# Kernel optimization log

Hardware: AMD Instinct MI355X
Metric: run time of the kernel (lower is better)

## Reference

```python
import jax, jax.numpy as jnp
import numpy as np

EMBED_DIM = 1024
HEADS = 16
HD = EMBED_DIM // HEADS

def setup_inputs() -> dict:
    key = jax.random.key(0)
    ks = jax.random.split(key, 6)
    s = 1.0 / np.sqrt(EMBED_DIM)
    x = jax.random.normal(ks[0], (4, 2048, EMBED_DIM), dtype=jnp.float32)
    Wq = jax.random.uniform(ks[1], (EMBED_DIM, EMBED_DIM), jnp.float32, -s, s)
    Wk = jax.random.uniform(ks[2], (EMBED_DIM, EMBED_DIM), jnp.float32, -s, s)
    Wv = jax.random.uniform(ks[3], (EMBED_DIM, EMBED_DIM), jnp.float32, -s, s)
    Wo = jax.random.uniform(ks[4], (EMBED_DIM, EMBED_DIM), jnp.float32, -s, s)
    bo = jax.random.uniform(ks[5], (EMBED_DIM,), jnp.float32, -s, s)
    return {"x": x, "Wq": Wq, "Wk": Wk, "Wv": Wv, "Wo": Wo, "bo": bo}

def reference(x, Wq, Wk, Wv, Wo, bo):
    B, S, E = x.shape
    # projections (torch Linear: y = x @ W.T), split into heads -> [B,H,S,hd]
    def proj(W):
        return (x @ W.T).reshape(B, S, HEADS, HD).transpose(0, 2, 1, 3)
    q, k, v = proj(Wq), proj(Wk), proj(Wv)
    energy = jnp.einsum('bhid,bhjd->bhij', q, k) / np.sqrt(HD).astype(np.float32)
    causal = jnp.tril(jnp.ones((S, S), dtype=bool))
    energy = jnp.where(causal, energy, -jnp.inf)
    attn = jax.nn.softmax(energy, axis=-1)  # dropout omitted (eval mode)
    out = jnp.einsum('bhij,bhjd->bhid', attn, v)
    out = out.transpose(0, 2, 1, 3).reshape(B, S, E)
    return out @ Wo.T + bo
```

## Files before the change

kernel.cpp:

```cpp
#include <hip/hip_runtime.h>
#include <math.h>

#define EMB   1024
#define HEADS 16
#define HD    64
#define SEQ   2048
#define BATCH 4
#define MTOT  (BATCH * SEQ)
#define XSZ   ((size_t)MTOT * EMB)
#define WSZ   ((size_t)EMB * EMB)

typedef __attribute__((ext_vector_type(8))) short s16x8;
typedef __attribute__((ext_vector_type(4))) short s16x4;
typedef __attribute__((ext_vector_type(4))) float f32x4;

__device__ __forceinline__ short f2bf(float f) {
    unsigned u = __builtin_bit_cast(unsigned, f);
    u += 0x7fffu + ((u >> 16) & 1u);
    return (short)(u >> 16);
}

__device__ __forceinline__ unsigned pk_bf16(float a, float b) {
#if __has_builtin(__builtin_amdgcn_cvt_pk_bf16_f32)
    typedef __attribute__((ext_vector_type(2))) __bf16 bf16x2;
    return __builtin_bit_cast(unsigned, __builtin_amdgcn_cvt_pk_bf16_f32(a, b));
#else
    return (unsigned)(unsigned short)f2bf(a) |
           ((unsigned)(unsigned short)f2bf(b) << 16);
#endif
}

__device__ __forceinline__ float fexp2(float x) {
#if __has_builtin(__builtin_amdgcn_exp2f)
    return __builtin_amdgcn_exp2f(x);
#else
    return exp2f(x);
#endif
}

__device__ __forceinline__ void async16(const void* g, void* l) {
    __builtin_amdgcn_global_load_lds(
        (const __attribute__((address_space(1))) unsigned*)g,
        (__attribute__((address_space(3))) unsigned*)l, 16, 0, 0);
}

__global__ __launch_bounds__(256)
void cvt_inputs(const float* __restrict__ x,  const float* __restrict__ wq,
                const float* __restrict__ wk, const float* __restrict__ wv,
                const float* __restrict__ wo, short* __restrict__ xb,
                short* __restrict__ wcat)
{
    const size_t e = ((size_t)blockIdx.x * 256 + threadIdx.x) * 8;
    const float* src;
    short* dst;
    float scale = 1.0f;
    if (e < XSZ) {
        src = x + e;
        dst = xb + e;
    } else {
        const size_t r = e - XSZ;
        const int w = (int)(r >> 20);
        const size_t off = r & (WSZ - 1);
        src = (w == 0 ? wq : w == 1 ? wk : w == 2 ? wv : wo) + off;
        dst = wcat + r;
        if (w == 0) scale = 0.125f * 1.44269504f;
    }
    const float4 a = ((const float4*)src)[0];
    const float4 b = ((const float4*)src)[1];
    s16x8 v;
    v[0] = f2bf(a.x * scale); v[1] = f2bf(a.y * scale);
    v[2] = f2bf(a.z * scale); v[3] = f2bf(a.w * scale);
    v[4] = f2bf(b.x * scale); v[5] = f2bf(b.y * scale);
    v[6] = f2bf(b.z * scale); v[7] = f2bf(b.w * scale);
    *(s16x8*)dst = v;
}

#define BAR() __builtin_amdgcn_s_barrier()
#define WAIT_LGKM() do { asm volatile("s_waitcnt lgkmcnt(0)" ::: "memory"); \
                         __builtin_amdgcn_sched_barrier(0); } while (0)
#define WAIT_VM(n) asm volatile("s_waitcnt vmcnt(" #n ")" ::: "memory")

#define RD_A4(bA) \
    _Pragma("unroll") for (int mi = 0; mi < 4; ++mi) \
    _Pragma("unroll") for (int kk = 0; kk < 2; ++kk) \
        a[mi][kk] = *(const s16x8*)((bA) + (wm4 + mi) * 2048 + kk * 1024 + abase);

#define RD_B2(bB, hf, breg) \
    _Pragma("unroll") for (int ni = 0; ni < 2; ++ni) \
    _Pragma("unroll") for (int kk = 0; kk < 2; ++kk) \
        breg[ni][kk] = *(const s16x8*)((bB) + (wn4 + (hf) * 2 + ni) * 2048 + kk * 1024 + abase);

#define MFMA16(hf, breg) \
    __builtin_amdgcn_s_setprio(1); \
    _Pragma("unroll") for (int mi = 0; mi < 4; ++mi) \
    _Pragma("unroll") for (int ni = 0; ni < 2; ++ni) \
    _Pragma("unroll") for (int kk = 0; kk < 2; ++kk) \
        acc[mi][(hf) * 2 + ni] = __builtin_amdgcn_mfma_f32_16x16x32_bf16( \
            a[mi][kk], breg[ni][kk], acc[mi][(hf) * 2 + ni], 0, 0, 0); \
    __builtin_amdgcn_s_setprio(0);

#define STA(pM, ldsM, h, k0) do { \
    async16((pM) + (size_t)((h) * 128) * K + (k0),      (ldsM) + (h) * 16384 + wv1024); \
    async16((pM) + (size_t)((h) * 128 + 64) * K + (k0), (ldsM) + (h) * 16384 + 8192 + wv1024); \
} while (0)

#define STB(pM, ldsM, k0) do { \
    async16((pM) + (k0),                (ldsM) + wv1024); \
    async16((pM) + (size_t)64 * K + (k0), (ldsM) + 8192 + wv1024); \
} while (0)

template<bool OUT_BF16>
__global__ __launch_bounds__(512, 2)
void gemm_qp(const short* __restrict__ A, const short* __restrict__ B,
             void* __restrict__ C, int ldc, const float* __restrict__ bias,
             int K, short* __restrict__ Vt)
{
    __shared__ __align__(16) char lds[147456];

    const int tid   = threadIdx.x;
    const int wv    = tid >> 6;
    const int lane  = tid & 63;
    const int col16 = lane & 15;
    const int quad  = lane >> 4;
    const int wm    = wv >> 1;
    const int wn    = wv & 1;
    const int wm4   = wm * 4;
    const int wn4   = wn * 4;
    const int wv1024 = wv << 10;

    const int nwg = gridDim.x * gridDim.y;
    int wg = blockIdx.y * gridDim.x + blockIdx.x;
    wg = (wg & 7) * (nwg >> 3) + (wg >> 3);
    const int rowBase = (wg / gridDim.x) * 256;
    const int colBase = (wg % gridDim.x) * 128;

    const int abase = (col16 * 64 + quad * 16) ^ ((col16 & 8) << 2);

    const int rlane = (lane >> 2) & 15;
    const int rw0   = ((wv >> 1) << 4) + rlane;
    const int colSt = ((wv & 1) << 5) + (((lane & 3) << 3) ^ ((lane & 32) >> 1));
    const short* pA = A + (size_t)(rowBase + rw0) * K + colSt;
    const short* pB = B + (size_t)(colBase + rw0) * K + colSt;

    s16x8 a[4][2], bq0[2][2], bq1[2][2];
    f32x4 acc[4][4];
#pragma unroll
    for (int i = 0; i < 4; ++i)
#pragma unroll
        for (int j = 0; j < 4; ++j) acc[i][j] = (f32x4){0.f, 0.f, 0.f, 0.f};

    const int NT = K >> 6;

    char* r0 = lds;
    char* r1 = lds + 49152;
    char* r2 = lds + 98304;

    STA(pA, r0, 0, 0);  STA(pA, r0, 1, 0);  STB(pB, r0 + 32768, 0);
    STA(pA, r1, 0, 64); STA(pA, r1, 1, 64); STB(pB, r1 + 32768, 64);
    WAIT_VM(6);
    BAR();

    for (int kt = 0; kt < NT; ++kt) {
        const int k0 = kt << 6;
        const bool more = (kt + 2 < NT);

        RD_A4(r0);
        RD_B2(r0 + 32768, 0, bq0);
        if (more) { STA(pA, r2, 0, k0 + 128); STB(pB, r2 + 32768, k0 + 128); }
        BAR(); WAIT_LGKM();
        MFMA16(0, bq0);
        BAR();

        RD_B2(r0 + 32768, 1, bq1);
        if (more) STA(pA, r2, 1, k0 + 128);
        BAR(); WAIT_LGKM();
        MFMA16(1, bq1);
        if (more) { WAIT_VM(6); } else { WAIT_VM(0); }
        BAR();

        char* t = r0; r0 = r1; r1 = r2; r2 = t;
    }

    if (OUT_BF16) {
        short* Cb = (short*)C;
        if (Vt != nullptr && colBase >= 2048) {
#pragma unroll
            for (int mi = 0; mi < 4; ++mi) {
                const int rg0 = rowBase + wm * 64 + mi * 16 + quad * 4;
                const int bq = rg0 >> 11;
                const int s0 = rg0 & 2047;
#pragma unroll
                for (int ni = 0; ni < 4; ++ni) {
                    const int cg2 = colBase - 2048 + wn * 64 + ni * 16 + col16;
                    const int hh = cg2 >> 6, dd = cg2 & 63;
                    short* dst = Vt + (((size_t)(bq * 16 + hh) * 64 + dd) << 11) + s0;
                    const f32x4 v = acc[mi][ni];
                    uint2 pw;
                    pw.x = pk_bf16(v[0], v[1]);
                    pw.y = pk_bf16(v[2], v[3]);
                    *(uint2*)dst = pw;
                }
            }
        } else {
#pragma unroll
            for (int mi = 0; mi < 4; ++mi) {
                const int rg0 = rowBase + wm * 64 + mi * 16 + quad * 4;
#pragma unroll
                for (int ni = 0; ni < 4; ++ni) {
                    const int cg = colBase + wn * 64 + ni * 16 + col16;
                    const f32x4 v = acc[mi][ni];
#pragma unroll
                    for (int r = 0; r < 4; ++r)
                        Cb[(size_t)(rg0 + r) * ldc + cg] = f2bf(v[r]);
                }
            }
        }
    } else {
        float* Cf = (float*)C;
#pragma unroll
        for (int ni = 0; ni < 4; ++ni) {
            const int cg = colBase + wn * 64 + ni * 16 + col16;
            const float bj = bias ? bias[cg] : 0.f;
#pragma unroll
            for (int mi = 0; mi < 4; ++mi) {
                const int rg0 = rowBase + wm * 64 + mi * 16 + quad * 4;
                const f32x4 v = acc[mi][ni];
#pragma unroll
                for (int r = 0; r < 4; ++r)
                    Cf[(size_t)(rg0 + r) * ldc + cg] = v[r] + bj;
            }
        }
    }
}

#define LDT 2048
__global__ __launch_bounds__(512)
void attn_mfma(const short* __restrict__ QK, const short* __restrict__ VT,
               short* __restrict__ O)
{
    __shared__ __align__(16) short lKV[4][2][64 * 64];
    __shared__ short lP[8 * 32 * 64];

    char* lPc = (char*)lP;

    const int tid  = threadIdx.x;
    const int wv   = tid >> 6;
    const int lane = tid & 63;
    const int col  = lane & 15;
    const int quad = lane >> 4;
    const int csw  = (col & 7) << 4;

    const int bh = blockIdx.y;
    const int b  = bh >> 4;
    const int h  = bh & 15;
    const size_t baseq = (size_t)b * SEQ * LDT + (size_t)h * HD;
    const size_t basek = baseq + 1024;
    const size_t baseo = (size_t)b * SEQ * EMB + (size_t)h * HD;
    const short* vtb = VT + ((size_t)bh << 17);

    const int srow   = tid >> 3;
    const int schunk = tid & 7;
    const int ssc    = (schunk ^ (srow & 7)) * 8;
    const int sdst   = srow * 128 + schunk * 16;

    char* pwv = lPc + wv * 4096;

    const s16x8 onesv = {0x3F80, 0x3F80, 0x3F80, 0x3F80,
                         0x3F80, 0x3F80, 0x3F80, 0x3F80};

#define STG(kt, bi) do { \
    async16(QK + basek + (size_t)((kt) * 64 + srow) * LDT + ssc, (char*)lKV[bi][0] + sdst); \
    async16(vtb + (size_t)srow * LDT + (kt) * 64 + ssc,          (char*)lKV[bi][1] + sdst); \
} while (0)

    for (int half = 0; half < 2; ++half) {
        const int qsuper = half ? (7 - (int)blockIdx.x) : (int)blockIdx.x;
        const int qb = qsuper * 256;
        const int qlo_w = qb + wv * 32;

        s16x8 qf[2][2];
#pragma unroll
        for (int rb = 0; rb < 2; ++rb) {
            const short* qr = QK + baseq + (size_t)(qlo_w + rb * 16 + col) * LDT;
            qf[rb][0] = *(const s16x8*)(qr + quad * 8);
            qf[rb][1] = *(const s16x8*)(qr + 32 + quad * 8);
        }

        f32x4 of[2][4], lsum[2];
#pragma unroll
        for (int rb = 0; rb < 2; ++rb) {
#pragma unroll
            for (int u = 0; u < 4; ++u) of[rb][u] = (f32x4){0.f, 0.f, 0.f, 0.f};
            lsum[rb] = (f32x4){0.f, 0.f, 0.f, 0.f};
        }

        const int nt = qb / 64 + 4;

        BAR();
        STG(0, 0);
        STG(1, 1);

        for (int kt = 0; kt < nt; ++kt) {
            const int kb = kt * 64;
            const int bi = kt & 3;
            if (kt + 2 < nt) STG(kt + 2, (kt + 2) & 3);
            const int rem = nt - 1 - kt;
            if (rem >= 2)      { WAIT_VM(4); }
            else if (rem == 1) { WAIT_VM(2); }
            else               { WAIT_VM(0); }
            BAR();

            if (kb > qlo_w + 31) continue;

            const char* lKb = (const char*)lKV[bi][0];
            const char* lVb = (const char*)lKV[bi][1];

            s16x8 kf[4][2];
#pragma unroll
            for (int t = 0; t < 4; ++t) {
                kf[t][0] = *(const s16x8*)(lKb + (t * 16 + col) * 128 + ((quad * 16) ^ csw));
                kf[t][1] = *(const s16x8*)(lKb + (t * 16 + col) * 128 + ((64 + quad * 16) ^ csw));
            }

#pragma unroll
            for (int rb = 0; rb < 2; ++rb) {
                const int qlo = qlo_w + rb * 16;
                const int qg  = qlo + col;

                f32x4 s[4];
#pragma unroll
                for (int t = 0; t < 4; ++t) {
                    f32x4 acc = (f32x4){0.f, 0.f, 0.f, 0.f};
                    acc = __builtin_amdgcn_mfma_f32_16x16x32_bf16(kf[t][0], qf[rb][0], acc, 0, 0, 0);
                    acc = __builtin_amdgcn_mfma_f32_16x16x32_bf16(kf[t][1], qf[rb][1], acc, 0, 0, 0);
                    s[t] = acc;
                }

                if (kb + 63 > qlo) {
#pragma unroll
                    for (int t = 0; t < 4; ++t)
#pragma unroll
                        for (int rr = 0; rr < 4; ++rr) {
                            const int kg = kb + t * 16 + quad * 4 + rr;
                            if (kg > qg) s[t][rr] = -3.0e38f;
                        }
                }

                char* pb = pwv + (rb * 16 + col) * 128;
#pragma unroll
                for (int t = 0; t < 4; ++t) {
                    uint2 pkd;
                    pkd.x = pk_bf16(fexp2(s[t][0]), fexp2(s[t][1]));
                    pkd.y = pk_bf16(fexp2(s[t][2]), fexp2(s[t][3]));
                    *(uint2*)(pb + ((t * 32 + quad * 8) ^ csw)) = pkd;
                }
            }

#pragma unroll
            for (int c = 0; c < 2; ++c) {
                s16x8 vf[4];
#pragma unroll
                for (int u = 0; u < 4; ++u)
                    vf[u] = *(const s16x8*)(lVb + (u * 16 + col) * 128 + ((c * 64 + quad * 16) ^ csw));
#pragma unroll
                for (int rb = 0; rb < 2; ++rb) {
                    const s16x8 pa = *(const s16x8*)(pwv + (rb * 16 + col) * 128 + ((c * 64 + quad * 16) ^ csw));
                    lsum[rb] = __builtin_amdgcn_mfma_f32_16x16x32_bf16(onesv, pa, lsum[rb], 0, 0, 0);
#pragma unroll
                    for (int u = 0; u < 4; ++u)
                        of[rb][u] = __builtin_amdgcn_mfma_f32_16x16x32_bf16(vf[u], pa, of[rb][u], 0, 0, 0);
                }
            }
        }

#pragma unroll
        for (int rb = 0; rb < 2; ++rb) {
            const float rl = 1.f / lsum[rb][0];
            short* orow = O + baseo + (size_t)(qlo_w + rb * 16 + col) * EMB + quad * 4;
#pragma unroll
            for (int u = 0; u < 4; ++u) {
                uint2 pkd;
                pkd.x = pk_bf16(of[rb][u][0] * rl, of[rb][u][1] * rl);
                pkd.y = pk_bf16(of[rb][u][2] * rl, of[rb][u][3] * rl);
                *(uint2*)&orow[u * 16] = pkd;
            }
        }
    }
#undef STG
}

extern "C" void kernel_launch(void* const* d_in, const int* in_sizes, int n_in,
                              void* d_out, int out_size, void* d_ws, size_t ws_size,
                              hipStream_t stream)
{
    const float* x  = (const float*)d_in[0];
    const float* Wq = (const float*)d_in[1];
    const float* Wk = (const float*)d_in[2];
    const float* Wv = (const float*)d_in[3];
    const float* Wo = (const float*)d_in[4];
    const float* bo = (const float*)d_in[5];
    float* out = (float*)d_out;

    short* xb   = (short*)d_ws;
    short* wcat = xb + XSZ;
    short* qk   = wcat + 4 * WSZ;
    short* vt   = qk + (size_t)MTOT * 2048;
    short* ob   = vt + (size_t)64 * 64 * 2048;

    const int cvt_blocks = (int)((XSZ + 4 * WSZ) / 8 / 256);
    cvt_inputs<<<cvt_blocks, 256, 0, stream>>>(x, Wq, Wk, Wv, Wo, xb, wcat);

    gemm_qp<true><<<dim3(3072 / 128, MTOT / 256), 512, 0, stream>>>(
        xb, wcat, qk, 2048, nullptr, EMB, vt);

    attn_mfma<<<dim3(4, BATCH * HEADS), 512, 0, stream>>>(qk, vt, ob);

    gemm_qp<false><<<dim3(EMB / 128, MTOT / 256), 512, 0, stream>>>(
        ob, wcat + (size_t)3 * WSZ, out, EMB, bo, EMB, nullptr);
}
```

Before: 243.9 us.

## Split QKV GEMM into small-LDS K32 kernel and halve attention query tile

Adds a dedicated QKV projection GEMM that uses a K-step of 32 with double buffering in 48KB of LDS instead of a triple-buffered 144KB layout, so more workgroups can be resident per CU. The output-projection GEMM keeps the old pipeline as its own kernel. The attention kernel now gives each wave 16 query rows instead of 32, doubles the grid to 8 blocks per head, and uses three rotating K/V LDS buffers with a simpler wait scheme. The aim is more occupancy and better load balance, at the cost of shorter MFMA runs, more barriers per K, and less K/V reuse across query rows.

```diff
diff --git a/kernel.cpp b/kernel.cpp
--- a/kernel.cpp
+++ b/kernel.cpp
@@ -80,42 +80,17 @@
                          __builtin_amdgcn_sched_barrier(0); } while (0)
 #define WAIT_VM(n) asm volatile("s_waitcnt vmcnt(" #n ")" ::: "memory")
 
-#define RD_A4(bA) \
-    _Pragma("unroll") for (int mi = 0; mi < 4; ++mi) \
-    _Pragma("unroll") for (int kk = 0; kk < 2; ++kk) \
-        a[mi][kk] = *(const s16x8*)((bA) + (wm4 + mi) * 2048 + kk * 1024 + abase);
-
-#define RD_B2(bB, hf, breg) \
-    _Pragma("unroll") for (int ni = 0; ni < 2; ++ni) \
-    _Pragma("unroll") for (int kk = 0; kk < 2; ++kk) \
-        breg[ni][kk] = *(const s16x8*)((bB) + (wn4 + (hf) * 2 + ni) * 2048 + kk * 1024 + abase);
-
-#define MFMA16(hf, breg) \
-    __builtin_amdgcn_s_setprio(1); \
-    _Pragma("unroll") for (int mi = 0; mi < 4; ++mi) \
-    _Pragma("unroll") for (int ni = 0; ni < 2; ++ni) \
-    _Pragma("unroll") for (int kk = 0; kk < 2; ++kk) \
-        acc[mi][(hf) * 2 + ni] = __builtin_amdgcn_mfma_f32_16x16x32_bf16( \
-            a[mi][kk], breg[ni][kk], acc[mi][(hf) * 2 + ni], 0, 0, 0); \
-    __builtin_amdgcn_s_setprio(0);
-
-#define STA(pM, ldsM, h, k0) do { \
-    async16((pM) + (size_t)((h) * 128) * K + (k0),      (ldsM) + (h) * 16384 + wv1024); \
-    async16((pM) + (size_t)((h) * 128 + 64) * K + (k0), (ldsM) + (h) * 16384 + 8192 + wv1024); \
+#define STG32(dst, k0) do { \
+    async16(pA32 + (k0),                     (dst) + wv1024); \
+    async16(pA32 + (size_t)128 * EMB + (k0), (dst) + 8192 + wv1024); \
+    async16(pB32 + (k0),                     (dst) + 16384 + wv1024); \
 } while (0)
 
-#define STB(pM, ldsM, k0) do { \
-    async16((pM) + (k0),                (ldsM) + wv1024); \
-    async16((pM) + (size_t)64 * K + (k0), (ldsM) + 8192 + wv1024); \
-} while (0)
-
-template<bool OUT_BF16>
 __global__ __launch_bounds__(512, 2)
-void gemm_qp(const short* __restrict__ A, const short* __restrict__ B,
-             void* __restrict__ C, int ldc, const float* __restrict__ bias,
-             int K, short* __restrict__ Vt)
+void gemm_qkv32(const short* __restrict__ A, const short* __restrict__ B,
+                short* __restrict__ C, int ldc, short* __restrict__ Vt)
 {
-    __shared__ __align__(16) char lds[147456];
+    __shared__ __align__(16) char lds[49152];
 
     const int tid   = threadIdx.x;
     const int wv    = tid >> 6;
@@ -137,6 +112,141 @@
     const int abase = (col16 * 64 + quad * 16) ^ ((col16 & 8) << 2);
 
     const int rlane = (lane >> 2) & 15;
+    const int colSt = ((lane & 3) << 3) ^ ((lane & 32) >> 1);
+    const short* pA32 = A + (size_t)(rowBase + wv * 16 + rlane) * EMB + colSt;
+    const short* pB32 = B + (size_t)(colBase + wv * 16 + rlane) * EMB + colSt;
+
+    s16x8 a[4], bq[4];
+    f32x4 acc[4][4];
+#pragma unroll
+    for (int i = 0; i < 4; ++i)
+#pragma unroll
+        for (int j = 0; j < 4; ++j) acc[i][j] = (f32x4){0.f, 0.f, 0.f, 0.f};
+
+    char* cb = lds;
+    char* nb = lds + 24576;
+
+    STG32(cb, 0);
+
+    for (int kt = 0; kt < 32; ++kt) {
+        const int k0 = kt << 5;
+        const bool more = (kt + 1 < 32);
+
+        if (more) STG32(nb, k0 + 32);
+        if (more) { WAIT_VM(3); } else { WAIT_VM(0); }
+        BAR();
+
+#pragma unroll
+        for (int mi = 0; mi < 4; ++mi)
+            a[mi] = *(const s16x8*)(cb + (wm4 + mi) * 1024 + abase);
+#pragma unroll
+        for (int ni = 0; ni < 4; ++ni)
+            bq[ni] = *(const s16x8*)(cb + 16384 + (wn4 + ni) * 1024 + abase);
+        WAIT_LGKM();
+
+        __builtin_amdgcn_s_setprio(1);
+#pragma unroll
+        for (int mi = 0; mi < 4; ++mi)
+#pragma unroll
+            for (int ni = 0; ni < 4; ++ni)
+                acc[mi][ni] = __builtin_amdgcn_mfma_f32_16x16x32_bf16(
+                    a[mi], bq[ni], acc[mi][ni], 0, 0, 0);
+        __builtin_amdgcn_s_setprio(0);
+        BAR();
+
+        char* t = cb; cb = nb; nb = t;
+    }
+
+    if (colBase >= 2048) {
+#pragma unroll
+        for (int mi = 0; mi < 4; ++mi) {
+            const int rg0 = rowBase + wm * 64 + mi * 16 + quad * 4;
+            const int bq_ = rg0 >> 11;
+            const int s0 = rg0 & 2047;
+#pragma unroll
+            for (int ni = 0; ni < 4; ++ni) {
+                const int cg2 = colBase - 2048 + wn * 64 + ni * 16 + col16;
+                const int hh = cg2 >> 6, dd = cg2 & 63;
+                short* dst = Vt + (((size_t)(bq_ * 16 + hh) * 64 + dd) << 11) + s0;
+                const f32x4 v = acc[mi][ni];
+                uint2 pw;
+                pw.x = pk_bf16(v[0], v[1]);
+                pw.y = pk_bf16(v[2], v[3]);
+                *(uint2*)dst = pw;
+            }
+        }
+    } else {
+#pragma unroll
+        for (int mi = 0; mi < 4; ++mi) {
+            const int rg0 = rowBase + wm * 64 + mi * 16 + quad * 4;
+#pragma unroll
+            for (int ni = 0; ni < 4; ++ni) {
+                const int cg = colBase + wn * 64 + ni * 16 + col16;
+                const f32x4 v = acc[mi][ni];
+#pragma unroll
+                for (int r = 0; r < 4; ++r)
+                    C[(size_t)(rg0 + r) * ldc + cg] = f2bf(v[r]);
+            }
+        }
+    }
+}
+
+#define RD_A4(bA) \
+    _Pragma("unroll") for (int mi = 0; mi < 4; ++mi) \
+    _Pragma("unroll") for (int kk = 0; kk < 2; ++kk) \
+        a[mi][kk] = *(const s16x8*)((bA) + (wm4 + mi) * 2048 + kk * 1024 + abase);
+
+#define RD_B2(bB, hf, breg) \
+    _Pragma("unroll") for (int ni = 0; ni < 2; ++ni) \
+    _Pragma("unroll") for (int kk = 0; kk < 2; ++kk) \
+        breg[ni][kk] = *(const s16x8*)((bB) + (wn4 + (hf) * 2 + ni) * 2048 + kk * 1024 + abase);
+
+#define MFMA16(hf, breg) \
+    __builtin_amdgcn_s_setprio(1); \
+    _Pragma("unroll") for (int mi = 0; mi < 4; ++mi) \
+    _Pragma("unroll") for (int ni = 0; ni < 2; ++ni) \
+    _Pragma("unroll") for (int kk = 0; kk < 2; ++kk) \
+        acc[mi][(hf) * 2 + ni] = __builtin_amdgcn_mfma_f32_16x16x32_bf16( \
+            a[mi][kk], breg[ni][kk], acc[mi][(hf) * 2 + ni], 0, 0, 0); \
+    __builtin_amdgcn_s_setprio(0);
+
+#define STA(pM, ldsM, h, k0) do { \
+    async16((pM) + (size_t)((h) * 128) * K + (k0),      (ldsM) + (h) * 16384 + wv1024); \
+    async16((pM) + (size_t)((h) * 128 + 64) * K + (k0), (ldsM) + (h) * 16384 + 8192 + wv1024); \
+} while (0)
+
+#define STB(pM, ldsM, k0) do { \
+    async16((pM) + (k0),                (ldsM) + wv1024); \
+    async16((pM) + (size_t)64 * K + (k0), (ldsM) + 8192 + wv1024); \
+} while (0)
+
+__global__ __launch_bounds__(512, 2)
+void gemm_out(const short* __restrict__ A, const short* __restrict__ B,
+              float* __restrict__ C, int ldc, const float* __restrict__ bias,
+              int K)
+{
+    __shared__ __align__(16) char lds[147456];
+
+    const int tid   = threadIdx.x;
+    const int wv    = tid >> 6;
+    const int lane  = tid & 63;
+    const int col16 = lane & 15;
+    const int quad  = lane >> 4;
+    const int wm    = wv >> 1;
+    const int wn    = wv & 1;
+    const int wm4   = wm * 4;
+    const int wn4   = wn * 4;
+    const int wv1024 = wv << 10;
+
+    const int nwg = gridDim.x * gridDim.y;
+    int wg = blockIdx.y * gridDim.x + blockIdx.x;
+    wg = (wg & 7) * (nwg >> 3) + (wg >> 3);
+    const int rowBase = (wg / gridDim.x) * 256;
+    const int colBase = (wg % gridDim.x) * 128;
+
+    const int abase = (col16 * 64 + quad * 16) ^ ((col16 & 8) << 2);
+
+    const int rlane = (lane >> 2) & 15;
     const int rw0   = ((wv >> 1) << 4) + rlane;
     const int colSt = ((wv & 1) << 5) + (((lane & 3) << 3) ^ ((lane & 32) >> 1));
     const short* pA = A + (size_t)(rowBase + rw0) * K + colSt;
@@ -181,54 +291,17 @@
         char* t = r0; r0 = r1; r1 = r2; r2 = t;
     }
 
-    if (OUT_BF16) {
-        short* Cb = (short*)C;
-        if (Vt != nullptr && colBase >= 2048) {
-#pragma unroll
-            for (int mi = 0; mi < 4; ++mi) {
-                const int rg0 = rowBase + wm * 64 + mi * 16 + quad * 4;
-                const int bq = rg0 >> 11;
-                const int s0 = rg0 & 2047;
-#pragma unroll
-                for (int ni = 0; ni < 4; ++ni) {
-                    const int cg2 = colBase - 2048 + wn * 64 + ni * 16 + col16;
-                    const int hh = cg2 >> 6, dd = cg2 & 63;
-                    short* dst = Vt + (((size_t)(bq * 16 + hh) * 64 + dd) << 11) + s0;
-                    const f32x4 v = acc[mi][ni];
-                    uint2 pw;
-                    pw.x = pk_bf16(v[0], v[1]);
-                    pw.y = pk_bf16(v[2], v[3]);
-                    *(uint2*)dst = pw;
-                }
-            }
-        } else {
-#pragma unroll
-            for (int mi = 0; mi < 4; ++mi) {
-                const int rg0 = rowBase + wm * 64 + mi * 16 + quad * 4;
-#pragma unroll
-                for (int ni = 0; ni < 4; ++ni) {
-                    const int cg = colBase + wn * 64 + ni * 16 + col16;
-                    const f32x4 v = acc[mi][ni];
-#pragma unroll
-                    for (int r = 0; r < 4; ++r)
-                        Cb[(size_t)(rg0 + r) * ldc + cg] = f2bf(v[r]);
-                }
-            }
-        }
-    } else {
-        float* Cf = (float*)C;
-#pragma unroll
-        for (int ni = 0; ni < 4; ++ni) {
-            const int cg = colBase + wn * 64 + ni * 16 + col16;
-            const float bj = bias ? bias[cg] : 0.f;
-#pragma unroll
-            for (int mi = 0; mi < 4; ++mi) {
-                const int rg0 = rowBase + wm * 64 + mi * 16 + quad * 4;
-                const f32x4 v = acc[mi][ni];
-#pragma unroll
-                for (int r = 0; r < 4; ++r)
-                    Cf[(size_t)(rg0 + r) * ldc + cg] = v[r] + bj;
-            }
+#pragma unroll
+    for (int ni = 0; ni < 4; ++ni) {
+        const int cg = colBase + wn * 64 + ni * 16 + col16;
+        const float bj = bias ? bias[cg] : 0.f;
+#pragma unroll
+        for (int mi = 0; mi < 4; ++mi) {
+            const int rg0 = rowBase + wm * 64 + mi * 16 + quad * 4;
+            const f32x4 v = acc[mi][ni];
+#pragma unroll
+            for (int r = 0; r < 4; ++r)
+                C[(size_t)(rg0 + r) * ldc + cg] = v[r] + bj;
         }
     }
 }
@@ -238,8 +311,8 @@
 void attn_mfma(const short* __restrict__ QK, const short* __restrict__ VT,
                short* __restrict__ O)
 {
-    __shared__ __align__(16) short lKV[4][2][64 * 64];
-    __shared__ short lP[8 * 32 * 64];
+    __shared__ __align__(16) short lKV[3][2][64 * 64];
+    __shared__ __align__(16) short lP[8 * 16 * 64];
 
     char* lPc = (char*)lP;
 
@@ -250,6 +323,7 @@
     const int quad = lane >> 4;
     const int csw  = (col & 7) << 4;
 
+    const int qpair = (int)blockIdx.x;
     const int bh = blockIdx.y;
     const int b  = bh >> 4;
     const int h  = bh & 15;
@@ -263,80 +337,73 @@
     const int ssc    = (schunk ^ (srow & 7)) * 8;
     const int sdst   = srow * 128 + schunk * 16;
 
-    char* pwv = lPc + wv * 4096;
+    char* pwv = lPc + wv * 2048;
 
     const s16x8 onesv = {0x3F80, 0x3F80, 0x3F80, 0x3F80,
                          0x3F80, 0x3F80, 0x3F80, 0x3F80};
 
-#define STG(kt, bi) do { \
-    async16(QK + basek + (size_t)((kt) * 64 + srow) * LDT + ssc, (char*)lKV[bi][0] + sdst); \
-    async16(vtb + (size_t)srow * LDT + (kt) * 64 + ssc,          (char*)lKV[bi][1] + sdst); \
+#define STG(kt, bp) do { \
+    async16(QK + basek + (size_t)((kt) * 64 + srow) * LDT + ssc, (char*)((bp)[0]) + sdst); \
+    async16(vtb + (size_t)srow * LDT + (kt) * 64 + ssc,          (char*)((bp)[1]) + sdst); \
 } while (0)
 
     for (int half = 0; half < 2; ++half) {
-        const int qsuper = half ? (7 - (int)blockIdx.x) : (int)blockIdx.x;
-        const int qb = qsuper * 256;
-        const int qlo_w = qb + wv * 32;
-
-        s16x8 qf[2][2];
-#pragma unroll
-        for (int rb = 0; rb < 2; ++rb) {
-            const short* qr = QK + baseq + (size_t)(qlo_w + rb * 16 + col) * LDT;
-            qf[rb][0] = *(const s16x8*)(qr + quad * 8);
-            qf[rb][1] = *(const s16x8*)(qr + 32 + quad * 8);
-        }
-
-        f32x4 of[2][4], lsum[2];
-#pragma unroll
-        for (int rb = 0; rb < 2; ++rb) {
-#pragma unroll
-            for (int u = 0; u < 4; ++u) of[rb][u] = (f32x4){0.f, 0.f, 0.f, 0.f};
-            lsum[rb] = (f32x4){0.f, 0.f, 0.f, 0.f};
-        }
-
-        const int nt = qb / 64 + 4;
+        const int qx = half ? (15 - qpair) : qpair;
+        const int qb = qx * 128;
+        const int qlo_w = qb + wv * 16;
+
+        s16x8 qf[2];
+        {
+            const short* qr = QK + baseq + (size_t)(qlo_w + col) * LDT;
+            qf[0] = *(const s16x8*)(qr + quad * 8);
+            qf[1] = *(const s16x8*)(qr + 32 + quad * 8);
+        }
+
+        f32x4 of[4], lsum;
+#pragma unroll
+        for (int u = 0; u < 4; ++u) of[u] = (f32x4){0.f, 0.f, 0.f, 0.f};
+        lsum = (f32x4){0.f, 0.f, 0.f, 0.f};
+
+        const int nt = qb / 64 + 2;
+
+        short (*b0)[64 * 64] = lKV[0];
+        short (*b1)[64 * 64] = lKV[1];
+        short (*b2)[64 * 64] = lKV[2];
 
         BAR();
-        STG(0, 0);
-        STG(1, 1);
+        __builtin_amdgcn_sched_barrier(0);
+        STG(0, b0);
+        STG(1, b1);
 
         for (int kt = 0; kt < nt; ++kt) {
             const int kb = kt * 64;
-            const int bi = kt & 3;
-            if (kt + 2 < nt) STG(kt + 2, (kt + 2) & 3);
-            const int rem = nt - 1 - kt;
-            if (rem >= 2)      { WAIT_VM(4); }
-            else if (rem == 1) { WAIT_VM(2); }
-            else               { WAIT_VM(0); }
+            if (kt + 1 < nt) { WAIT_VM(2); } else { WAIT_VM(0); }
             BAR();
-
-            if (kb > qlo_w + 31) continue;
-
-            const char* lKb = (const char*)lKV[bi][0];
-            const char* lVb = (const char*)lKV[bi][1];
-
-            s16x8 kf[4][2];
-#pragma unroll
-            for (int t = 0; t < 4; ++t) {
-                kf[t][0] = *(const s16x8*)(lKb + (t * 16 + col) * 128 + ((quad * 16) ^ csw));
-                kf[t][1] = *(const s16x8*)(lKb + (t * 16 + col) * 128 + ((64 + quad * 16) ^ csw));
-            }
-
-#pragma unroll
-            for (int rb = 0; rb < 2; ++rb) {
-                const int qlo = qlo_w + rb * 16;
-                const int qg  = qlo + col;
+            __builtin_amdgcn_sched_barrier(0);
+            if (kt + 2 < nt) STG(kt + 2, b2);
+
+            if (kb <= qlo_w + 15) {
+                const char* lKb = (const char*)(b0[0]);
+                const char* lVb = (const char*)(b0[1]);
+
+                s16x8 kf[4][2];
+#pragma unroll
+                for (int t = 0; t < 4; ++t) {
+                    kf[t][0] = *(const s16x8*)(lKb + (t * 16 + col) * 128 + ((quad * 16) ^ csw));
+                    kf[t][1] = *(const s16x8*)(lKb + (t * 16 + col) * 128 + ((64 + quad * 16) ^ csw));
+                }
 
                 f32x4 s[4];
 #pragma unroll
                 for (int t = 0; t < 4; ++t) {
                     f32x4 acc = (f32x4){0.f, 0.f, 0.f, 0.f};
-                    acc = __builtin_amdgcn_mfma_f32_16x16x32_bf16(kf[t][0], qf[rb][0], acc, 0, 0, 0);
-                    acc = __builtin_amdgcn_mfma_f32_16x16x32_bf16(kf[t][1], qf[rb][1], acc, 0, 0, 0);
+                    acc = __builtin_amdgcn_mfma_f32_16x16x32_bf16(kf[t][0], qf[0], acc, 0, 0, 0);
+                    acc = __builtin_amdgcn_mfma_f32_16x16x32_bf16(kf[t][1], qf[1], acc, 0, 0, 0);
                     s[t] = acc;
                 }
 
-                if (kb + 63 > qlo) {
+                const int qg = qlo_w + col;
+                if (kb + 63 > qlo_w) {
 #pragma unroll
                     for (int t = 0; t < 4; ++t)
 #pragma unroll
@@ -346,7 +413,7 @@
                         }
                 }
 
-                char* pb = pwv + (rb * 16 + col) * 128;
+                char* pb = pwv + col * 128;
 #pragma unroll
                 for (int t = 0; t < 4; ++t) {
                     uint2 pkd;
@@ -354,36 +421,32 @@
                     pkd.y = pk_bf16(fexp2(s[t][2]), fexp2(s[t][3]));
                     *(uint2*)(pb + ((t * 32 + quad * 8) ^ csw)) = pkd;
                 }
-            }
-
-#pragma unroll
-            for (int c = 0; c < 2; ++c) {
-                s16x8 vf[4];
-#pragma unroll
-                for (int u = 0; u < 4; ++u)
-                    vf[u] = *(const s16x8*)(lVb + (u * 16 + col) * 128 + ((c * 64 + quad * 16) ^ csw));
-#pragma unroll
-                for (int rb = 0; rb < 2; ++rb) {
-                    const s16x8 pa = *(const s16x8*)(pwv + (rb * 16 + col) * 128 + ((c * 64 + quad * 16) ^ csw));
-                    lsum[rb] = __builtin_amdgcn_mfma_f32_16x16x32_bf16(onesv, pa, lsum[rb], 0, 0, 0);
+
+#pragma unroll
+                for (int c = 0; c < 2; ++c) {
+                    s16x8 vf[4];
 #pragma unroll
                     for (int u = 0; u < 4; ++u)
-                        of[rb][u] = __builtin_amdgcn_mfma_f32_16x16x32_bf16(vf[u], pa, of[rb][u], 0, 0, 0);
+                        vf[u] = *(const s16x8*)(lVb + (u * 16 + col) * 128 + ((c * 64 + quad * 16) ^ csw));
+                    const s16x8 pa = *(const s16x8*)(pwv + col * 128 + ((c * 64 + quad * 16) ^ csw));
+                    lsum = __builtin_amdgcn_mfma_f32_16x16x32_bf16(onesv, pa, lsum, 0, 0, 0);
+#pragma unroll
+                    for (int u = 0; u < 4; ++u)
+                        of[u] = __builtin_amdgcn_mfma_f32_16x16x32_bf16(vf[u], pa, of[u], 0, 0, 0);
                 }
             }
-        }
-
-#pragma unroll
-        for (int rb = 0; rb < 2; ++rb) {
-            const float rl = 1.f / lsum[rb][0];
-            short* orow = O + baseo + (size_t)(qlo_w + rb * 16 + col) * EMB + quad * 4;
-#pragma unroll
-            for (int u = 0; u < 4; ++u) {
-                uint2 pkd;
-                pkd.x = pk_bf16(of[rb][u][0] * rl, of[rb][u][1] * rl);
-                pkd.y = pk_bf16(of[rb][u][2] * rl, of[rb][u][3] * rl);
-                *(uint2*)&orow[u * 16] = pkd;
-            }
+
+            short (*tmp)[64 * 64] = b0; b0 = b1; b1 = b2; b2 = tmp;
+        }
+
+        const float rl = 1.f / lsum[0];
+        short* orow = O + baseo + (size_t)(qlo_w + col) * EMB + quad * 4;
+#pragma unroll
+        for (int u = 0; u < 4; ++u) {
+            uint2 pkd;
+            pkd.x = pk_bf16(of[u][0] * rl, of[u][1] * rl);
+            pkd.y = pk_bf16(of[u][2] * rl, of[u][3] * rl);
+            *(uint2*)&orow[u * 16] = pkd;
         }
     }
 #undef STG
@@ -410,11 +473,11 @@
     const int cvt_blocks = (int)((XSZ + 4 * WSZ) / 8 / 256);
     cvt_inputs<<<cvt_blocks, 256, 0, stream>>>(x, Wq, Wk, Wv, Wo, xb, wcat);
 
-    gemm_qp<true><<<dim3(3072 / 128, MTOT / 256), 512, 0, stream>>>(
-        xb, wcat, qk, 2048, nullptr, EMB, vt);
-
-    attn_mfma<<<dim3(4, BATCH * HEADS), 512, 0, stream>>>(qk, vt, ob);
-
-    gemm_qp<false><<<dim3(EMB / 128, MTOT / 256), 512, 0, stream>>>(
-        ob, wcat + (size_t)3 * WSZ, out, EMB, bo, EMB, nullptr);
-}
+    gemm_qkv32<<<dim3(3072 / 128, MTOT / 256), 512, 0, stream>>>(
+        xb, wcat, qk, 2048, vt);
+
+    attn_mfma<<<dim3(8, BATCH * HEADS), 512, 0, stream>>>(qk, vt, ob);
+
+    gemm_out<<<dim3(EMB / 128, MTOT / 256), 512, 0, stream>>>(
+        ob, wcat + (size_t)3 * WSZ, out, EMB, bo, EMB);
+}
```

Measured after the change: 230.3 us. -5.6%, faster.
